# Performance work log

Measured on AMD Instinct MI355X. Metric: run time of the kernel, lower is better.

Reference implementation:

```python
import jax, jax.numpy as jnp
import numpy as np

B, N = 128, 2048
DX = 10.0 / 2048.0   # X / N
DT = 5.0e-4          # CFL-consistent timestep


def f_real(u):
    # f(u) = 0.5*u*(3 - u^2) + (300/12)*u^2*(3/4 - 2u + 3/2 u^2 - 1/4 u^4)
    u2 = u * u
    return 0.5 * u * (3.0 - u2) + 25.0 * u2 * (0.75 - 2.0 * u + 1.5 * u2 - 0.25 * u2 * u2)


def dfdu_abs(u):
    # f_real is elementwise, so grad of the sum gives the elementwise derivative,
    # matching torch.autograd.grad(f, u, grad_outputs=ones_like(f))
    return jnp.abs(jax.grad(lambda uu: jnp.sum(f_real(uu)))(u))


def setup_inputs() -> dict:
    key = jax.random.key(0)
    init = jax.random.uniform(key, (B, N), dtype=jnp.float32)  # u in [0,1]
    return {"init": init, "stepnum": 500}


def reference(init, stepnum):
    lam = jnp.float32(DT / DX)

    def step(u_old, _):
        f = f_real(u_old)                      # [B, N]
        a = dfdu_abs(u_old)                    # |f'(u)|, [B, N]
        # local Lax-Friedrichs flux: max over the (j, j+1) pair
        alpha = jnp.maximum(a[:, :-1], a[:, 1:])  # [B, N-1]
        f_half = 0.5 * (f[:, :-1] + f[:, 1:]) - 0.5 * alpha * (u_old[:, 1:] - u_old[:, :-1])
        interior = u_old[:, 1:-1] - lam * (f_half[:, 1:] - f_half[:, :-1])  # [B, N-2]
        # boundary: u[:,0]=u[:,1], u[:,N-1]=u[:,N-2]
        u = jnp.concatenate([interior[:, :1], interior, interior[:, -1:]], axis=1)
        return u, u

    _, traj = jax.lax.scan(step, init, None, length=stepnum - 1)  # [stepnum-1, B, N]
    return jnp.concatenate([init[None], traj], axis=0)            # [stepnum, B, N]
```

## Files before the change

### kernel.cpp

```cpp
#include <hip/hip_runtime.h>

#define NPTS   2048
#define TPB    576
#define WIN    1152
#define TCHUNK 125

typedef float v2f __attribute__((ext_vector_type(2)));

#define EDGE_BARRIER() do {                                   \
    asm volatile("s_waitcnt lgkmcnt(0)" ::: "memory");        \
    __builtin_amdgcn_s_barrier();                             \
    asm volatile("" ::: "memory");                            \
} while (0)

__device__ __forceinline__ v2f s2(float x) { v2f v; v.x = x; v.y = x; return v; }

__device__ __forceinline__ v2f fma2(v2f a, v2f b, v2f c) {
#if __has_builtin(__builtin_elementwise_fma)
    return __builtin_elementwise_fma(a, b, c);
#else
    v2f r; r.x = fmaf(a.x, b.x, c.x); r.y = fmaf(a.y, b.y, c.y); return r;
#endif
}

__device__ __forceinline__ void eval_gq2(v2f u, v2f& g, v2f& q) {
    const v2f uu = u * u;
    v2f gg = fma2(uu, s2(-3.125f), s2(18.75f));
    gg = fma2(u, gg, s2(-25.25f));
    gg = fma2(u, gg, s2(9.375f));
    gg = fma2(u, gg, s2(0.75f));
    g = u * gg;
    v2f pp = fma2(uu, s2(-37.5f), s2(150.0f));
    pp = fma2(u, pp, s2(-151.5f));
    pp = fma2(u, pp, s2(37.5f));
    v2f p = fma2(u, pp, s2(1.5f));
    v2f ap; ap.x = fabsf(p.x); ap.y = fabsf(p.y);
    q = ap * s2(0.5f);
}

__global__ __launch_bounds__(TPB) void lxf_tc(
    const float* __restrict__ srcrow, float* __restrict__ out,
    int nbatch, int t0, int nsub, int copy0)
{
    __shared__ float Ub[2][WIN];
    __shared__ float Gb[2][WIN];
    __shared__ float Qb[2][WIN];

    const int blk = blockIdx.x;
    const int r   = blk >> 1;
    const int h   = blk & 1;
    const int tid = threadIdx.x;
    const int c0  = 2 * tid;
    const int wb  = h ? (NPTS - WIN) : 0;
    const float lam = 0.1024f;

    const bool st  = h ? (c0 >= 128) : (c0 < 1024);
    const bool bcL = (h == 0) && (tid == 0);
    const bool bcR = (h == 1) && (tid == TPB - 1);
    const int  hl  = (tid == 0)       ? 0       : c0 - 1;
    const int  hr  = (tid == TPB - 1) ? WIN - 1 : c0 + 2;
    const int dist = h ? (125 - c0) : (c0 - 1025);

    v2f uv = *reinterpret_cast<const v2f*>(srcrow + (size_t)r * NPTS + wb + c0);
    v2f gv, qv;
    eval_gq2(uv, gv, qv);

    const size_t stride = (size_t)nbatch * NPTS;
    float* sp = out + (size_t)t0 * stride + (size_t)r * NPTS + (wb + c0);
    if (copy0 && st) *reinterpret_cast<v2f*>(sp) = uv;

    *reinterpret_cast<v2f*>(&Ub[0][c0]) = uv;
    *reinterpret_cast<v2f*>(&Gb[0][c0]) = gv;
    *reinterpret_cast<v2f*>(&Qb[0][c0]) = qv;
    EDGE_BARRIER();

    float* dstw = sp;
    int rem = nsub - 1;

#define STEP(CUR, NXT) do {                                              \
    dstw += stride;                                                      \
    if (dist <= rem) {                                                   \
        const float uL = Ub[CUR][hl], gL = Gb[CUR][hl], qL = Qb[CUR][hl];\
        const float uR = Ub[CUR][hr], gR = Gb[CUR][hr], qR = Qb[CUR][hr];\
        const float aL = fmaxf(qL, qv.x);                                \
        const float aM = fmaxf(qv.x, qv.y);                              \
        const float aR = fmaxf(qv.y, qR);                                \
        const float fhL = fmaf(-aL, uv.x - uL, gL + gv.x);               \
        const float fhM = fmaf(-aM, uv.y - uv.x, gv.x + gv.y);           \
        const float fhR = fmaf(-aR, uR - uv.y, gv.y + gR);               \
        float n0 = fmaf(-lam, fhM - fhL, uv.x);                          \
        float n1 = fmaf(-lam, fhR - fhM, uv.y);                          \
        if (bcL) n0 = n1;                           \
        if (bcR) n1 = n0;                           \
        uv.x = n0; uv.y = n1;                                            \
        eval_gq2(uv, gv, qv);                                            \
        *reinterpret_cast<v2f*>(&Ub[NXT][c0]) = uv;                      \
        *reinterpret_cast<v2f*>(&Gb[NXT][c0]) = gv;                      \
        *reinterpret_cast<v2f*>(&Qb[NXT][c0]) = qv;                      \
        if (st) *reinterpret_cast<v2f*>(dstw) = uv;                      \
    }                                                                    \
    --rem;                                                               \
    EDGE_BARRIER();                                                      \
} while (0)

    const int P2 = nsub >> 1;
    for (int i = 0; i < P2; ++i) {
        STEP(0, 1);
        STEP(1, 0);
    }
    if (nsub & 1) STEP(0, 1);
#undef STEP
}

extern "C" void kernel_launch(void* const* d_in, const int* in_sizes, int n_in,
                              void* d_out, int out_size, void* d_ws, size_t ws_size,
                              hipStream_t stream) {
    const float* init = (const float*)d_in[0];
    float* out = (float*)d_out;

    const int nbatch = in_sizes[0] / NPTS;
    const int nsteps = out_size / in_sizes[0];
    const int S = nsteps - 1;
    const size_t stride = (size_t)nbatch * NPTS;

    int t0 = 0;
    int first = 1;
    while (t0 < S) {
        int nsub = S - t0;
        if (nsub > TCHUNK) nsub = TCHUNK;
        const float* srcrow = first ? init : (out + (size_t)t0 * stride);
        hipLaunchKernelGGL(lxf_tc, dim3(2 * nbatch), dim3(TPB), 0, stream,
                           srcrow, out, nbatch, t0, nsub, first);
        t0 += nsub;
        first = 0;
    }
}
```

Measured before the change: 170.8 us.

## Split each row into four overlapping windows with smaller blocks

Each batch row is now handled by four blocks of 384 threads, each owning a 768-point window with 128-point halos, instead of two blocks of 576 threads with 1152-point windows. The per-step skip of work outside the dependency cone is dropped, and neighbor loads become aligned 2-float LDS reads. The stored derivative is now raw p, with abs and the 0.5 factor applied at use. The aim is more blocks for better CU occupancy and cheaper LDS access, at the cost of more redundant halo computation per row and some extra ALU work per step.

```diff
diff --git a/kernel.cpp b/kernel.cpp
--- a/kernel.cpp
+++ b/kernel.cpp
@@ -1,8 +1,8 @@
 #include <hip/hip_runtime.h>
 
 #define NPTS   2048
-#define TPB    576
-#define WIN    1152
+#define TPB    384
+#define WIN    768
 #define TCHUNK 125
 
 typedef float v2f __attribute__((ext_vector_type(2)));
@@ -23,7 +23,7 @@
 #endif
 }
 
-__device__ __forceinline__ void eval_gq2(v2f u, v2f& g, v2f& q) {
+__device__ __forceinline__ void eval_gp2(v2f u, v2f& g, v2f& p) {
     const v2f uu = u * u;
     v2f gg = fma2(uu, s2(-3.125f), s2(18.75f));
     gg = fma2(u, gg, s2(-25.25f));
@@ -33,73 +33,73 @@
     v2f pp = fma2(uu, s2(-37.5f), s2(150.0f));
     pp = fma2(u, pp, s2(-151.5f));
     pp = fma2(u, pp, s2(37.5f));
-    v2f p = fma2(u, pp, s2(1.5f));
-    v2f ap; ap.x = fabsf(p.x); ap.y = fabsf(p.y);
-    q = ap * s2(0.5f);
+    p = fma2(u, pp, s2(1.5f));
 }
 
-__global__ __launch_bounds__(TPB) void lxf_tc(
+__global__ __launch_bounds__(TPB) void lxf_tc4(
     const float* __restrict__ srcrow, float* __restrict__ out,
     int nbatch, int t0, int nsub, int copy0)
 {
     __shared__ float Ub[2][WIN];
     __shared__ float Gb[2][WIN];
-    __shared__ float Qb[2][WIN];
+    __shared__ float Pb[2][WIN];
 
     const int blk = blockIdx.x;
-    const int r   = blk >> 1;
-    const int h   = blk & 1;
+    const int r   = blk >> 2;
+    const int h   = blk & 3;
     const int tid = threadIdx.x;
     const int c0  = 2 * tid;
-    const int wb  = h ? (NPTS - WIN) : 0;
+    const int wb  = (h == 0) ? 0 : ((h == 1) ? 384 : ((h == 2) ? 896 : 1280));
+    const int own_lo = 512 * h - wb;
     const float lam = 0.1024f;
 
-    const bool st  = h ? (c0 >= 128) : (c0 < 1024);
+    const bool st  = (c0 >= own_lo) && (c0 < own_lo + 512);
     const bool bcL = (h == 0) && (tid == 0);
-    const bool bcR = (h == 1) && (tid == TPB - 1);
-    const int  hl  = (tid == 0)       ? 0       : c0 - 1;
-    const int  hr  = (tid == TPB - 1) ? WIN - 1 : c0 + 2;
-    const int dist = h ? (125 - c0) : (c0 - 1025);
-
-    v2f uv = *reinterpret_cast<const v2f*>(srcrow + (size_t)r * NPTS + wb + c0);
-    v2f gv, qv;
-    eval_gq2(uv, gv, qv);
+    const bool bcR = (h == 3) && (tid == TPB - 1);
+    const int  il  = (tid == 0)       ? 0       : c0 - 2;
+    const int  ir  = (tid == TPB - 1) ? WIN - 2 : c0 + 2;
 
     const size_t stride = (size_t)nbatch * NPTS;
+    v2f uv = *reinterpret_cast<const v2f*>(srcrow + (size_t)r * NPTS + wb + c0);
+    v2f gv, pv;
+    eval_gp2(uv, gv, pv);
+
     float* sp = out + (size_t)t0 * stride + (size_t)r * NPTS + (wb + c0);
     if (copy0 && st) *reinterpret_cast<v2f*>(sp) = uv;
 
     *reinterpret_cast<v2f*>(&Ub[0][c0]) = uv;
     *reinterpret_cast<v2f*>(&Gb[0][c0]) = gv;
-    *reinterpret_cast<v2f*>(&Qb[0][c0]) = qv;
+    *reinterpret_cast<v2f*>(&Pb[0][c0]) = pv;
     EDGE_BARRIER();
 
     float* dstw = sp;
-    int rem = nsub - 1;
 
 #define STEP(CUR, NXT) do {                                              \
     dstw += stride;                                                      \
-    if (dist <= rem) {                                                   \
-        const float uL = Ub[CUR][hl], gL = Gb[CUR][hl], qL = Qb[CUR][hl];\
-        const float uR = Ub[CUR][hr], gR = Gb[CUR][hr], qR = Qb[CUR][hr];\
-        const float aL = fmaxf(qL, qv.x);                                \
-        const float aM = fmaxf(qv.x, qv.y);                              \
-        const float aR = fmaxf(qv.y, qR);                                \
-        const float fhL = fmaf(-aL, uv.x - uL, gL + gv.x);               \
-        const float fhM = fmaf(-aM, uv.y - uv.x, gv.x + gv.y);           \
-        const float fhR = fmaf(-aR, uR - uv.y, gv.y + gR);               \
-        float n0 = fmaf(-lam, fhM - fhL, uv.x);                          \
-        float n1 = fmaf(-lam, fhR - fhM, uv.y);                          \
-        if (bcL) n0 = n1;                           \
-        if (bcR) n1 = n0;                           \
-        uv.x = n0; uv.y = n1;                                            \
-        eval_gq2(uv, gv, qv);                                            \
-        *reinterpret_cast<v2f*>(&Ub[NXT][c0]) = uv;                      \
-        *reinterpret_cast<v2f*>(&Gb[NXT][c0]) = gv;                      \
-        *reinterpret_cast<v2f*>(&Qb[NXT][c0]) = qv;                      \
-        if (st) *reinterpret_cast<v2f*>(dstw) = uv;                      \
-    }                                                                    \
-    --rem;                                                               \
+    const v2f uLp = *reinterpret_cast<const v2f*>(&Ub[CUR][il]);         \
+    const v2f uRp = *reinterpret_cast<const v2f*>(&Ub[CUR][ir]);         \
+    const v2f gLp = *reinterpret_cast<const v2f*>(&Gb[CUR][il]);         \
+    const v2f gRp = *reinterpret_cast<const v2f*>(&Gb[CUR][ir]);         \
+    const v2f pLp = *reinterpret_cast<const v2f*>(&Pb[CUR][il]);         \
+    const v2f pRp = *reinterpret_cast<const v2f*>(&Pb[CUR][ir]);         \
+    const float uL = uLp.y, gL = gLp.y, pL = pLp.y;                      \
+    const float uR = uRp.x, gR = gRp.x, pR = pRp.x;                      \
+    const float aL = fmaxf(fabsf(pL), fabsf(pv.x));                      \
+    const float aM = fmaxf(fabsf(pv.x), fabsf(pv.y));                    \
+    const float aR = fmaxf(fabsf(pv.y), fabsf(pR));                      \
+    const float fhL = fmaf(-0.5f * aL, uv.x - uL, gL + gv.x);            \
+    const float fhM = fmaf(-0.5f * aM, uv.y - uv.x, gv.x + gv.y);        \
+    const float fhR = fmaf(-0.5f * aR, uR - uv.y, gv.y + gR);            \
+    float n0 = fmaf(-lam, fhM - fhL, uv.x);                              \
+    float n1 = fmaf(-lam, fhR - fhM, uv.y);                              \
+    if (bcL) n0 = n1;                               \
+    if (bcR) n1 = n0;                               \
+    uv.x = n0; uv.y = n1;                                                \
+    eval_gp2(uv, gv, pv);                                                \
+    *reinterpret_cast<v2f*>(&Ub[NXT][c0]) = uv;                          \
+    *reinterpret_cast<v2f*>(&Gb[NXT][c0]) = gv;                          \
+    *reinterpret_cast<v2f*>(&Pb[NXT][c0]) = pv;                          \
+    if (st) *reinterpret_cast<v2f*>(dstw) = uv;                          \
     EDGE_BARRIER();                                                      \
 } while (0)
 
@@ -129,7 +129,7 @@
         int nsub = S - t0;
         if (nsub > TCHUNK) nsub = TCHUNK;
         const float* srcrow = first ? init : (out + (size_t)t0 * stride);
-        hipLaunchKernelGGL(lxf_tc, dim3(2 * nbatch), dim3(TPB), 0, stream,
+        hipLaunchKernelGGL(lxf_tc4, dim3(4 * nbatch), dim3(TPB), 0, stream,
                            srcrow, out, nbatch, t0, nsub, first);
         t0 += nsub;
         first = 0;
```

Measured after the change: 183.0 us. +7.2%, slower.
